# Performance work log

Hardware: AMD Instinct MI355X
Metric: run time of the kernel (lower is better)

Reference implementation:

```python
import jax, jax.numpy as jnp
import numpy as np

HIDDEN_DIM = 512
RADIUS = 128


def rel_pos_indexes(seq_len_q: int, seq_len_k: int, radius: int):
    # (i - j) clamped to [-radius, radius], shifted to [0, 2*radius]
    i = jnp.arange(seq_len_k)[None, :]   # [1, Sk]
    j = jnp.arange(seq_len_q)[:, None]   # [Sq, 1]
    return jnp.clip(i - j, -radius, radius) + radius  # [Sq, Sk] int


def setup_inputs() -> dict:
    key = jax.random.key(0)
    kq, kk, kv, ke = jax.random.split(key, 4)
    B, Sq, Sk, d = 4, 2048, 2048, HIDDEN_DIM
    Q = jax.random.normal(kq, (B, Sq, d), dtype=jnp.float32)
    K = jax.random.normal(kk, (B, Sk, d), dtype=jnp.float32)
    V = jax.random.normal(kv, (B, Sk, d), dtype=jnp.float32)
    # learned relative-position embedding table: (2R+1, d)
    rel_embeds = jax.random.normal(ke, (2 * RADIUS + 1, d), dtype=jnp.float32)
    return {"Q": Q, "K": K, "V": V, "rel_embeds": rel_embeds}


def reference(Q, K, V, rel_embeds):
    B, Sq, d = Q.shape
    Sk = K.shape[1]
    normalizer = jnp.asarray(d ** 0.5, dtype=Q.dtype)
    # content scores: [B, Sq, Sk]
    energy = jnp.einsum('bqd,bkd->bqk', Q, K)
    # relative scores: Q against the (2R+1) relative embeddings -> [B, Sq, 2R+1]
    Q_rel = jnp.einsum('bqd,rd->bqr', Q, rel_embeds)
    idx = rel_pos_indexes(Sq, Sk, RADIUS)  # [Sq, Sk]
    # gather along last dim per query row (same index map for every batch)
    rel_shift = jnp.take_along_axis(Q_rel, idx[None, :, :].repeat(B, axis=0), axis=2)
    energy = (energy + rel_shift) / normalizer
    attn = jax.nn.softmax(energy, axis=2)
    Z = jnp.einsum('bqk,bkd->bqd', attn, V)
    return attn, Z
```

## Files before the change

### kernel.cpp

```cpp
#include <hip/hip_runtime.h>

#define BATCH 4
#define SQL 2048
#define SKL 2048
#define DIM 512
#define NR 257
#define NRP 288
#define RAD 128

typedef __bf16 bf16x8 __attribute__((ext_vector_type(8)));
typedef float f32x4 __attribute__((ext_vector_type(4)));
typedef unsigned short u16;
typedef u16 u16x4 __attribute__((ext_vector_type(4)));
typedef u16 u16x8 __attribute__((ext_vector_type(8)));

__device__ inline u16 f2bf(float x) {
  union { float f; unsigned u; } v; v.f = x;
  unsigned r = v.u + 0x7FFF + ((v.u >> 16) & 1);
  return (u16)(r >> 16);
}

__device__ inline void glds16(const u16* g, const u16* l) {
  __builtin_amdgcn_global_load_lds(
      (const __attribute__((address_space(1))) void*)g,
      (__attribute__((address_space(3))) void*)l, 16, 0, 0);
}

__global__ __launch_bounds__(256) void prep_mem_kernel(const float* __restrict__ Q,
                                                       const float* __restrict__ K,
                                                       const float* __restrict__ V,
                                                       const float* __restrict__ rel,
                                                       u16x4* __restrict__ Qb,
                                                       u16x4* __restrict__ Kb,
                                                       u16* __restrict__ relb,
                                                       u16* __restrict__ Vt) {
  __shared__ float tile[32][33];
  int bid = blockIdx.x, tid = threadIdx.x;
  if (bid < 8192) {
    const f32x4* src = (bid < 4096) ? (const f32x4*)Q : (const f32x4*)K;
    u16x4* dst = (bid < 4096) ? Qb : Kb;
    int i = (bid & 4095) * 256 + tid;
    f32x4 f = src[i];
    u16x4 o;
#pragma unroll
    for (int e = 0; e < 4; e++) o[e] = f2bf(f[e]);
    dst[i] = o;
  } else if (bid < 8768) {
    int i = (bid - 8192) * 256 + tid;
    int r = i >> 9;
    relb[i] = (r < NR) ? f2bf(rel[i]) : (u16)0;
  } else {
    int t = bid - 8768;
    int b = t >> 10, rem = t & 1023;
    int k0 = (rem & 63) * 32, d0 = (rem >> 6) * 32;
    int tx = tid & 31, ty = tid >> 5;
#pragma unroll
    for (int r = 0; r < 4; r++)
      tile[ty + r * 8][tx] = V[((long)b * SKL + k0 + ty + r * 8) * DIM + d0 + tx];
    __syncthreads();
#pragma unroll
    for (int r = 0; r < 4; r++)
      Vt[((long)b * DIM + d0 + ty + r * 8) * SKL + k0 + tx] = f2bf(tile[tx][ty + r * 8]);
  }
}

__global__ __launch_bounds__(256) void qrel_kernel(const u16* __restrict__ Qb,
                                                   const u16* __restrict__ relb,
                                                   float* __restrict__ Qrel) {
  int tid = threadIdx.x;
  int wave = tid >> 6, lane = tid & 63;
  int m0 = blockIdx.x * 64 + wave * 16;
  int j0 = blockIdx.y * 2;
  int fr = lane & 15, fk = (lane >> 4) * 8;
  f32x4 acc[2] = {};
  const u16* qrow = Qb + (long)(m0 + fr) * DIM + fk;
  const u16* r0 = relb + (long)(j0 * 16 + fr) * DIM + fk;
  const u16* r1 = r0 + 16 * DIM;
  for (int k0 = 0; k0 < DIM; k0 += 32) {
    bf16x8 a = *(const bf16x8*)(qrow + k0);
    bf16x8 b0 = *(const bf16x8*)(r0 + k0);
    bf16x8 b1 = *(const bf16x8*)(r1 + k0);
    acc[0] = __builtin_amdgcn_mfma_f32_16x16x32_bf16(a, b0, acc[0], 0, 0, 0);
    acc[1] = __builtin_amdgcn_mfma_f32_16x16x32_bf16(a, b1, acc[1], 0, 0, 0);
  }
  int cr = (lane >> 4) * 4, cc = lane & 15;
#pragma unroll
  for (int t = 0; t < 2; t++)
#pragma unroll
    for (int r = 0; r < 4; r++)
      Qrel[(long)(m0 + cr + r) * NRP + (j0 + t) * 16 + cc] = acc[t][r];
}

__global__ __launch_bounds__(512, 2) void energy_kernel(const u16* __restrict__ Qb,
                                                        const u16* __restrict__ Kb,
                                                        u16* __restrict__ S) {
  __shared__ u16 lds[65536];
  int b = blockIdx.z;
  int m0 = blockIdx.y * 256, n0 = blockIdx.x * 256;
  const u16* A = Qb + (long)b * SQL * DIM;
  const u16* Bp = Kb + (long)b * SKL * DIM;
  int tid = threadIdx.x;
  int wave = tid >> 6, lane = tid & 63;
  int wr = wave >> 2, wc = wave & 3;
  int fr = lane & 15, g = lane >> 4;
  int srow8 = lane >> 3;
  int scol = ((lane & 7) ^ srow8) * 8;

  f32x4 acc[4][2][4] = {};
  bf16x8 bB[4][2];

#define STA(slot, tt, q) do { \
    int rb_ = (q) * 32 + (wave & 3) * 8 + (wave >> 2) * 128; \
    glds16(A + (long)(m0 + rb_ + srow8) * DIM + (tt) * 64 + scol, \
           lds + (slot) * 32768 + rb_ * 64); \
  } while (0)
#define STB(slot, tt, p) do { \
    int rb_ = (p) * 64 + wave * 8; \
    glds16(Bp + (long)(n0 + rb_ + srow8) * DIM + (tt) * 64 + scol, \
           lds + (slot) * 32768 + 16384 + rb_ * 64); \
  } while (0)
#define LOADB(slot) do { \
    const u16* base_ = lds + (slot) * 32768 + 16384; \
    _Pragma("unroll") for (int jb = 0; jb < 4; jb++) { \
      _Pragma("unroll") for (int ks = 0; ks < 2; ks++) { \
        int row_ = wc * 64 + jb * 16 + fr; \
        int cb_ = (ks * 64 + g * 16) ^ ((row_ & 7) << 4); \
        bB[jb][ks] = *(const bf16x8*)(base_ + row_ * 64 + (cb_ >> 1)); \
      } \
    } \
  } while (0)
#define QUAD(slot, q) do { \
    const u16* baseA_ = lds + (slot) * 32768; \
    bf16x8 a_[2][2]; \
    _Pragma("unroll") for (int rb = 0; rb < 2; rb++) { \
      _Pragma("unroll") for (int ks = 0; ks < 2; ks++) { \
        int row_ = wr * 128 + (q) * 32 + rb * 16 + fr; \
        int cb_ = (ks * 64 + g * 16) ^ ((row_ & 7) << 4); \
        a_[rb][ks] = *(const bf16x8*)(baseA_ + row_ * 64 + (cb_ >> 1)); \
      } \
    } \
    __builtin_amdgcn_s_setprio(1); \
    _Pragma("unroll") for (int rb = 0; rb < 2; rb++) \
    _Pragma("unroll") for (int jb = 0; jb < 4; jb++) \
    _Pragma("unroll") for (int ks = 0; ks < 2; ks++) \
      acc[q][rb][jb] = __builtin_amdgcn_mfma_f32_16x16x32_bf16(a_[rb][ks], bB[jb][ks], acc[q][rb][jb], 0, 0, 0); \
    __builtin_amdgcn_s_setprio(0); \
  } while (0)

  const int NT = DIM / 64;
  STA(0, 0, 0); STA(0, 0, 1); STA(0, 0, 2); STA(0, 0, 3);
  STB(0, 0, 0); STB(0, 0, 1); STB(0, 0, 2); STB(0, 0, 3);
  STA(1, 1, 0); STA(1, 1, 1); STA(1, 1, 2);
  asm volatile("s_waitcnt vmcnt(3)" ::: "memory");
  asm volatile("s_barrier" ::: "memory");

  for (int t = 0; t < NT; ++t) {
    int cs = t & 1, ns = cs ^ 1;
    if (t + 1 < NT) {
      STA(ns, t + 1, 3);
      STB(ns, t + 1, 0); STB(ns, t + 1, 1); STB(ns, t + 1, 2); STB(ns, t + 1, 3);
    }
    LOADB(cs);
    QUAD(cs, 0);
    asm volatile("s_barrier" ::: "memory");
    if (t + 2 < NT) STA(cs, t + 2, 0);
    QUAD(cs, 1);
    asm volatile("s_barrier" ::: "memory");
    if (t + 2 < NT) STA(cs, t + 2, 1);
    QUAD(cs, 2);
    asm volatile("s_barrier" ::: "memory");
    if (t + 2 < NT) STA(cs, t + 2, 2);
    QUAD(cs, 3);
    if (t + 2 < NT) asm volatile("s_waitcnt vmcnt(3)" ::: "memory");
    else            asm volatile("s_waitcnt vmcnt(0)" ::: "memory");
    asm volatile("s_barrier" ::: "memory");
  }
#undef STA
#undef STB
#undef LOADB
#undef QUAD

  const float inv_norm = 0.04419417382415922f;
  int cr = (lane >> 4) * 4, cc = lane & 15;
#pragma unroll
  for (int q = 0; q < 4; q++)
#pragma unroll
    for (int rb = 0; rb < 2; rb++)
#pragma unroll
      for (int r = 0; r < 4; r++) {
        int row = m0 + wr * 128 + q * 32 + rb * 16 + cr + r;
        u16* sr = S + ((long)b * SQL + row) * SKL;
#pragma unroll
        for (int jb = 0; jb < 4; jb++)
          sr[n0 + wc * 64 + jb * 16 + cc] = f2bf(acc[q][rb][jb][r] * inv_norm);
      }
}

__global__ __launch_bounds__(256) void softmax_kernel(u16* __restrict__ S,
                                                      const float* __restrict__ Qrel,
                                                      float* __restrict__ attn) {
  long row = blockIdx.x;
  int q = (int)(row & (SQL - 1));
  u16* srow = S + row * SKL;
  float* arow = attn + row * SKL;
  int tid = threadIdx.x;
  int wave = tid >> 6, lane = tid & 63;
  __shared__ float qlds[NR];
  __shared__ float red[4];
  const float inv_norm = 0.04419417382415922f;
  const float* qr = Qrel + row * NRP;
  qlds[tid] = qr[tid] * inv_norm;
  if (tid == 0) qlds[256] = qr[256] * inv_norm;
  bf16x8 v = *(const bf16x8*)(srow + tid * 8);
  __syncthreads();
  float f[8];
  int kb = tid * 8 - q + RAD;
#pragma unroll
  for (int e = 0; e < 8; e++) {
    int idx = kb + e;
    idx = idx < 0 ? 0 : (idx > 2 * RAD ? 2 * RAD : idx);
    f[e] = (float)v[e] + qlds[idx];
  }
  float m = -1e30f;
#pragma unroll
  for (int e = 0; e < 8; e++) m = fmaxf(m, f[e]);
  for (int o = 32; o > 0; o >>= 1) m = fmaxf(m, __shfl_xor(m, o));
  if (lane == 0) red[wave] = m;
  __syncthreads();
  m = fmaxf(fmaxf(red[0], red[1]), fmaxf(red[2], red[3]));
  __syncthreads();
  float s = 0.0f;
  float e8[8];
#pragma unroll
  for (int e = 0; e < 8; e++) { e8[e] = __expf(f[e] - m); s += e8[e]; }
  for (int o = 32; o > 0; o >>= 1) s += __shfl_xor(s, o);
  if (lane == 0) red[wave] = s;
  __syncthreads();
  s = red[0] + red[1] + red[2] + red[3];
  float inv = 1.0f / s;
  f32x4 o0, o1;
  u16x8 pb;
#pragma unroll
  for (int e = 0; e < 4; e++) {
    float p = e8[e] * inv;
    o0[e] = p; pb[e] = f2bf(p);
  }
#pragma unroll
  for (int e = 0; e < 4; e++) {
    float p = e8[e + 4] * inv;
    o1[e] = p; pb[e + 4] = f2bf(p);
  }
  *(f32x4*)(arow + tid * 8) = o0;
  *(f32x4*)(arow + tid * 8 + 4) = o1;
  *(u16x8*)(srow + tid * 8) = pb;
}

__global__ __launch_bounds__(256) void z_kernel(const u16* __restrict__ S,
                                                const u16* __restrict__ Vt,
                                                float* __restrict__ Z) {
  int b = blockIdx.z;
  int m0 = blockIdx.y * 64;
  int n0 = blockIdx.x * 128;
  const u16* A = S + (long)b * SQL * SKL;
  const u16* Bp = Vt + (long)b * DIM * SKL;
  __shared__ u16 lds[24576];
  u16* As0 = lds;          u16* Bs0 = lds + 4096;
  u16* As1 = lds + 12288;  u16* Bs1 = lds + 16384;
  int tid = threadIdx.x;
  int wave = tid >> 6, lane = tid & 63;
  int wm = (wave >> 1) * 32, wn = (wave & 1) * 64;
  int fr = lane & 15, g = lane >> 4;
  int srow = lane >> 3;
  int scol = ((lane & 7) ^ srow) * 8;
  f32x4 acc[2][4] = {};

  auto stage = [&](u16* dA, u16* dB, int k0) {
#pragma unroll
    for (int c = 0; c < 2; c++) {
      int r = wave * 16 + c * 8;
      glds16(A + (long)(m0 + r + srow) * SKL + k0 + scol, dA + r * 64);
    }
#pragma unroll
    for (int c = 0; c < 4; c++) {
      int r = wave * 32 + c * 8;
      glds16(Bp + (long)(n0 + r + srow) * SKL + k0 + scol, dB + r * 64);
    }
  };
  auto compute = [&](const u16* Asb, const u16* Bsb) {
#pragma unroll
    for (int s = 0; s < 2; s++) {
      bf16x8 af[2], bfv[4];
#pragma unroll
      for (int i = 0; i < 2; i++) {
        int row = wm + i * 16 + fr;
        int cb = (s * 64 + g * 16) ^ ((row & 7) << 4);
        af[i] = *(const bf16x8*)(Asb + row * 64 + (cb >> 1));
      }
#pragma unroll
      for (int j = 0; j < 4; j++) {
        int row = wn + j * 16 + fr;
        int cb = (s * 64 + g * 16) ^ ((row & 7) << 4);
        bfv[j] = *(const bf16x8*)(Bsb + row * 64 + (cb >> 1));
      }
#pragma unroll
      for (int i = 0; i < 2; i++)
#pragma unroll
        for (int j = 0; j < 4; j++)
          acc[i][j] = __builtin_amdgcn_mfma_f32_16x16x32_bf16(af[i], bfv[j], acc[i][j], 0, 0, 0);
    }
  };

  const int NT = SKL / 64;
  stage(As0, Bs0, 0);
  __syncthreads();
  for (int t = 0; t < NT; t += 2) {
    if (t + 1 < NT) stage(As1, Bs1, (t + 1) * 64);
    compute(As0, Bs0);
    __syncthreads();
    if (t + 1 < NT) {
      if (t + 2 < NT) stage(As0, Bs0, (t + 2) * 64);
      compute(As1, Bs1);
      __syncthreads();
    }
  }

  int cr = (lane >> 4) * 4, cc = lane & 15;
#pragma unroll
  for (int i = 0; i < 2; i++)
#pragma unroll
    for (int r = 0; r < 4; r++) {
      int q = m0 + wm + i * 16 + cr + r;
      float* zrow = Z + ((long)b * SQL + q) * DIM;
#pragma unroll
      for (int j = 0; j < 4; j++)
        zrow[n0 + wn + j * 16 + cc] = acc[i][j][r];
    }
}


extern "C" void kernel_launch(void* const* d_in, const int* in_sizes, int n_in,
                              void* d_out, int out_size, void* d_ws, size_t ws_size,
                              hipStream_t stream) {
  const float* Q = (const float*)d_in[0];
  const float* K = (const float*)d_in[1];
  const float* V = (const float*)d_in[2];
  const float* rel = (const float*)d_in[3];
  float* attn = (float*)d_out;
  float* Z = attn + (long)BATCH * SQL * SKL;

  char* ws = (char*)d_ws;
  u16* Qb   = (u16*)ws;
  u16* Kb   = (u16*)(ws + 8388608);
  u16* Vt   = (u16*)(ws + 16777216);
  u16* relb = (u16*)(ws + 25165824);
  float* Qrel = (float*)(ws + 25460736);
  u16* S    = (u16*)(ws + 34897920);

  prep_mem_kernel<<<12864, 256, 0, stream>>>(Q, K, V, rel, (u16x4*)Qb, (u16x4*)Kb, relb, Vt);
  qrel_kernel<<<dim3(128, 9), 256, 0, stream>>>(Qb, relb, Qrel);
  energy_kernel<<<dim3(8, 8, BATCH), 512, 0, stream>>>(Qb, Kb, S);
  softmax_kernel<<<8192, 256, 0, stream>>>(S, Qrel, attn);
  z_kernel<<<dim3(4, 32, BATCH), 256, 0, stream>>>(S, Vt, Z);
}
```

Measured before the change: 225.1 us.

## Restructure Z GEMM to 128x128 tiles with 8 waves and explicit prefetch pipeline

The attn·V kernel now uses 512-thread blocks computing 128x128 output tiles instead of 64x128, halving the grid. LDS fragments are loaded into registers before the barrier so the stage two tiles ahead can be issued into the just-freed buffer while MFMAs run. Hand-placed waitcnt/barrier instructions and s_setprio replace __syncthreads. This raises per-block reuse of A/B tiles and overlap of loads with compute, at the cost of more registers and fewer blocks (256 total) for occupancy.

```diff
diff --git a/kernel.cpp b/kernel.cpp
--- a/kernel.cpp
+++ b/kernel.cpp
@@ -255,85 +255,90 @@
   *(u16x8*)(srow + tid * 8) = pb;
 }
 
-__global__ __launch_bounds__(256) void z_kernel(const u16* __restrict__ S,
-                                                const u16* __restrict__ Vt,
-                                                float* __restrict__ Z) {
+__global__ __launch_bounds__(512, 4) void z_kernel(const u16* __restrict__ S,
+                                                   const u16* __restrict__ Vt,
+                                                   float* __restrict__ Z) {
+  __shared__ u16 lds[32768];
   int b = blockIdx.z;
-  int m0 = blockIdx.y * 64;
+  int m0 = blockIdx.y * 128;
   int n0 = blockIdx.x * 128;
   const u16* A = S + (long)b * SQL * SKL;
   const u16* Bp = Vt + (long)b * DIM * SKL;
-  __shared__ u16 lds[24576];
-  u16* As0 = lds;          u16* Bs0 = lds + 4096;
-  u16* As1 = lds + 12288;  u16* Bs1 = lds + 16384;
   int tid = threadIdx.x;
   int wave = tid >> 6, lane = tid & 63;
-  int wm = (wave >> 1) * 32, wn = (wave & 1) * 64;
+  int wr = wave >> 2, wc = wave & 3;
   int fr = lane & 15, g = lane >> 4;
-  int srow = lane >> 3;
-  int scol = ((lane & 7) ^ srow) * 8;
-  f32x4 acc[2][4] = {};
-
-  auto stage = [&](u16* dA, u16* dB, int k0) {
-#pragma unroll
-    for (int c = 0; c < 2; c++) {
-      int r = wave * 16 + c * 8;
-      glds16(A + (long)(m0 + r + srow) * SKL + k0 + scol, dA + r * 64);
-    }
-#pragma unroll
-    for (int c = 0; c < 4; c++) {
-      int r = wave * 32 + c * 8;
-      glds16(Bp + (long)(n0 + r + srow) * SKL + k0 + scol, dB + r * 64);
-    }
-  };
-  auto compute = [&](const u16* Asb, const u16* Bsb) {
-#pragma unroll
-    for (int s = 0; s < 2; s++) {
-      bf16x8 af[2], bfv[4];
-#pragma unroll
-      for (int i = 0; i < 2; i++) {
-        int row = wm + i * 16 + fr;
-        int cb = (s * 64 + g * 16) ^ ((row & 7) << 4);
-        af[i] = *(const bf16x8*)(Asb + row * 64 + (cb >> 1));
+  int srow8 = lane >> 3;
+  int scol = ((lane & 7) ^ srow8) * 8;
+
+  f32x4 acc[4][2] = {};
+
+#define ZSTG(slot, tt) do { \
+    _Pragma("unroll") for (int i_ = 0; i_ < 2; i_++) { \
+      int r_ = wave * 16 + i_ * 8; \
+      glds16(A + (long)(m0 + r_ + srow8) * SKL + (tt) * 64 + scol, \
+             lds + (slot) * 16384 + r_ * 64); \
+      glds16(Bp + (long)(n0 + r_ + srow8) * SKL + (tt) * 64 + scol, \
+             lds + (slot) * 16384 + 8192 + r_ * 64); \
+    } \
+  } while (0)
+
+  const int NT = SKL / 64;
+  ZSTG(0, 0);
+  ZSTG(1, 1);
+  asm volatile("s_waitcnt vmcnt(4)" ::: "memory");
+  asm volatile("s_barrier" ::: "memory");
+
+  for (int t = 0; t < NT; ++t) {
+    int cs = t & 1;
+    const u16* baseA = lds + cs * 16384;
+    const u16* baseB = lds + cs * 16384 + 8192;
+    bf16x8 aF[4][2], bF[2][2];
+#pragma unroll
+    for (int rb = 0; rb < 4; rb++)
+#pragma unroll
+      for (int ks = 0; ks < 2; ks++) {
+        int row = wr * 64 + rb * 16 + fr;
+        int cb = (ks * 64 + g * 16) ^ ((row & 7) << 4);
+        aF[rb][ks] = *(const bf16x8*)(baseA + row * 64 + (cb >> 1));
       }
 #pragma unroll
-      for (int j = 0; j < 4; j++) {
-        int row = wn + j * 16 + fr;
-        int cb = (s * 64 + g * 16) ^ ((row & 7) << 4);
-        bfv[j] = *(const bf16x8*)(Bsb + row * 64 + (cb >> 1));
+    for (int jb = 0; jb < 2; jb++)
+#pragma unroll
+      for (int ks = 0; ks < 2; ks++) {
+        int row = wc * 32 + jb * 16 + fr;
+        int cb = (ks * 64 + g * 16) ^ ((row & 7) << 4);
+        bF[jb][ks] = *(const bf16x8*)(baseB + row * 64 + (cb >> 1));
       }
-#pragma unroll
-      for (int i = 0; i < 2; i++)
-#pragma unroll
-        for (int j = 0; j < 4; j++)
-          acc[i][j] = __builtin_amdgcn_mfma_f32_16x16x32_bf16(af[i], bfv[j], acc[i][j], 0, 0, 0);
-    }
-  };
-
-  const int NT = SKL / 64;
-  stage(As0, Bs0, 0);
-  __syncthreads();
-  for (int t = 0; t < NT; t += 2) {
-    if (t + 1 < NT) stage(As1, Bs1, (t + 1) * 64);
-    compute(As0, Bs0);
-    __syncthreads();
-    if (t + 1 < NT) {
-      if (t + 2 < NT) stage(As0, Bs0, (t + 2) * 64);
-      compute(As1, Bs1);
-      __syncthreads();
-    }
-  }
+    asm volatile("s_waitcnt lgkmcnt(0)" ::: "memory");
+    __builtin_amdgcn_sched_barrier(0);
+    asm volatile("s_barrier" ::: "memory");
+    if (t + 2 < NT) ZSTG(cs, t + 2);
+    __builtin_amdgcn_s_setprio(1);
+#pragma unroll
+    for (int rb = 0; rb < 4; rb++)
+#pragma unroll
+      for (int jb = 0; jb < 2; jb++)
+#pragma unroll
+        for (int ks = 0; ks < 2; ks++)
+          acc[rb][jb] = __builtin_amdgcn_mfma_f32_16x16x32_bf16(aF[rb][ks], bF[jb][ks], acc[rb][jb], 0, 0, 0);
+    __builtin_amdgcn_s_setprio(0);
+    if (t + 2 < NT) asm volatile("s_waitcnt vmcnt(4)" ::: "memory");
+    else            asm volatile("s_waitcnt vmcnt(0)" ::: "memory");
+    asm volatile("s_barrier" ::: "memory");
+  }
+#undef ZSTG
 
   int cr = (lane >> 4) * 4, cc = lane & 15;
 #pragma unroll
-  for (int i = 0; i < 2; i++)
+  for (int rb = 0; rb < 4; rb++)
 #pragma unroll
     for (int r = 0; r < 4; r++) {
-      int q = m0 + wm + i * 16 + cr + r;
+      int q = m0 + wr * 64 + rb * 16 + cr + r;
       float* zrow = Z + ((long)b * SQL + q) * DIM;
 #pragma unroll
-      for (int j = 0; j < 4; j++)
-        zrow[n0 + wn + j * 16 + cc] = acc[i][j][r];
+      for (int jb = 0; jb < 2; jb++)
+        zrow[n0 + wc * 32 + jb * 16 + cc] = acc[rb][jb][r];
     }
 }
 
@@ -360,5 +365,5 @@
   qrel_kernel<<<dim3(128, 9), 256, 0, stream>>>(Qb, relb, Qrel);
   energy_kernel<<<dim3(8, 8, BATCH), 512, 0, stream>>>(Qb, Kb, S);
   softmax_kernel<<<8192, 256, 0, stream>>>(S, Qrel, attn);
-  z_kernel<<<dim3(4, 32, BATCH), 256, 0, stream>>>(S, Vt, Z);
-}
+  z_kernel<<<dim3(4, 16, BATCH), 512, 0, stream>>>(S, Vt, Z);
+}
```

Measured after the change: 216.6 us. 1.04x faster.
